# Kernel optimization log

Hardware: AMD Instinct MI355X
Metric: run time of the kernel (lower is better)

## Reference

```python
import jax, jax.numpy as jnp
import numpy as np

N_NEWS, N_ENT, N_TOP = 100000, 50000, 2000
D = 128
N_EDGES = 1600000
HID, OUT = 512, 128


def setup_inputs() -> dict:
    key = jax.random.key(0)
    ks = jax.random.split(key, 12)
    return {
        "news_feats": jax.random.normal(ks[0], (N_NEWS, D), jnp.float32),
        "entity_feats": jax.random.normal(ks[1], (N_ENT, D), jnp.float32),
        "topic_feats": jax.random.normal(ks[2], (N_TOP, D), jnp.float32),
        "ent_row": jax.random.randint(ks[3], (N_EDGES,), 0, N_NEWS, jnp.int32),
        "ent_col": jax.random.randint(ks[4], (N_EDGES,), 0, N_ENT, jnp.int32),
        "top_row": jax.random.randint(ks[5], (N_EDGES,), 0, N_NEWS, jnp.int32),
        "top_col": jax.random.randint(ks[6], (N_EDGES,), 0, N_TOP, jnp.int32),
        "W1": jax.random.normal(ks[7], (3 * D, HID), jnp.float32) * 0.05,
        "b1": jnp.zeros((HID,), jnp.float32),
        "W2": jax.random.normal(ks[8], (HID, OUT), jnp.float32) * 0.05,
        "b2": jnp.zeros((OUT,), jnp.float32),
    }


def _agg(feats, row, col, num_news):
    # SpMM with binary adjacency: sum neighbor feats per news node
    gathered = feats[col]                                   # [E, D]
    summed = jax.ops.segment_sum(gathered, row, num_segments=num_news)
    deg = jax.ops.segment_sum(jnp.ones_like(row, dtype=feats.dtype), row,
                              num_segments=num_news)
    return summed / (deg[:, None] + 1e-8)


def reference(news_feats, entity_feats, topic_feats, ent_row, ent_col,
              top_row, top_col, W1, b1, W2, b2):
    n = news_feats.shape[0]
    ent_agg = _agg(entity_feats, ent_row, ent_col, n)
    top_agg = _agg(topic_feats, top_row, top_col, n)
    out = jnp.concatenate([news_feats, ent_agg, top_agg], axis=1)  # [N, 3D]
    h = jnp.tanh(out @ W1 + b1)
    return h @ W2 + b2
```

## Files before the change

kernel.cpp:

```cpp
#include <hip/hip_runtime.h>
#include <hip/hip_bf16.h>

#define NN 100000
#define NE 50000
#define NT 2000
#define DD 128
#define NEDGE 1600000
#define HID 512
#define OUTD 128
#define K1 (3*DD)
#define NBKT 391

typedef __bf16 bf16x8 __attribute__((ext_vector_type(8)));
typedef __bf16 bf16x4 __attribute__((ext_vector_type(4)));
typedef float  f32x4  __attribute__((ext_vector_type(4)));

__device__ __forceinline__ __bf16 f2b(float f) {
    __hip_bfloat16 h = __float2bfloat16(f);
    union { __hip_bfloat16 h; __bf16 b; } u; u.h = h; return u.b;
}

__device__ __forceinline__ void gll16(const void* g, void* l) {
    __builtin_amdgcn_global_load_lds((const __attribute__((address_space(1))) void*)g,
                                     (__attribute__((address_space(3))) void*)l, 16, 0, 0);
}

__device__ __forceinline__ float ftanh(float x) {
    x = fminf(fmaxf(x, -15.f), 15.f);
    float t = __expf(2.f * x);
    return (t - 1.f) / (t + 1.f);
}

__global__ void conv_feats(const float* __restrict__ entf, const float* __restrict__ topf,
                           __bf16* __restrict__ entb, __bf16* __restrict__ topb) {
    long i = ((long)blockIdx.x * 256 + threadIdx.x) * 4;
    const long NEL = (long)NE * DD;
    if (i < NEL) {
        float4 v = *(const float4*)(entf + i);
        *(bf16x4*)(entb + i) = bf16x4{f2b(v.x), f2b(v.y), f2b(v.z), f2b(v.w)};
    } else {
        long j = i - NEL;
        float4 v = *(const float4*)(topf + j);
        *(bf16x4*)(topb + j) = bf16x4{f2b(v.x), f2b(v.y), f2b(v.z), f2b(v.w)};
    }
}

__global__ __launch_bounds__(256) void hist_buckets(const int* __restrict__ er,
                                                    const int* __restrict__ tr,
                                                    int* __restrict__ bc_e,
                                                    int* __restrict__ bc_t) {
    __shared__ int lhe[NBKT], lht[NBKT];
    const int tid = threadIdx.x;
    for (int i = tid; i < NBKT; i += 256) { lhe[i] = 0; lht[i] = 0; }
    __syncthreads();
    const int base = blockIdx.x * 8192;
    #pragma unroll 4
    for (int k = 0; k < 32; k++) {
        int e = base + k * 256 + tid;
        if (e < NEDGE) {
            atomicAdd(&lhe[er[e] >> 8], 1);
            atomicAdd(&lht[tr[e] >> 8], 1);
        }
    }
    __syncthreads();
    for (int i = tid; i < NBKT; i += 256) {
        if (lhe[i]) atomicAdd(&bc_e[i], lhe[i]);
        if (lht[i]) atomicAdd(&bc_t[i], lht[i]);
    }
}

__global__ void scan_buckets(int* __restrict__ bc_e, int* __restrict__ bc_t,
                             int* __restrict__ cur_e, int* __restrict__ cur_t,
                             int* __restrict__ offs_e, int* __restrict__ offs_t) {
    int* bc  = blockIdx.y ? bc_t : bc_e;
    int* cur = blockIdx.y ? cur_t : cur_e;
    int* offs = blockIdx.y ? offs_t : offs_e;
    __shared__ int s[512];
    int i = threadIdx.x;
    s[i] = (i < NBKT) ? bc[i] : 0;
    __syncthreads();
    #pragma unroll
    for (int off = 1; off < 512; off <<= 1) {
        int v = (i >= off) ? s[i - off] : 0;
        __syncthreads();
        s[i] += v;
        __syncthreads();
    }
    if (i < NBKT) {
        bc[i] = s[i];
        cur[i] = i ? s[i - 1] : 0;
    }
    if (i == 0) offs[0] = 0;
}

__global__ __launch_bounds__(256) void scatter_bucket(const int* __restrict__ er,
                                                      const int* __restrict__ ec,
                                                      const int* __restrict__ tr,
                                                      const int* __restrict__ tc,
                                                      int* __restrict__ cur_e,
                                                      int* __restrict__ cur_t,
                                                      int* __restrict__ be,
                                                      int* __restrict__ bt) {
    __shared__ int lhe[NBKT], lht[NBKT];
    __shared__ int lbe[NBKT], lbt[NBKT];
    const int tid = threadIdx.x;
    for (int i = tid; i < NBKT; i += 256) { lhe[i] = 0; lht[i] = 0; }
    __syncthreads();
    const int base = blockIdx.x * 4096;
    #pragma unroll 4
    for (int k = 0; k < 16; k++) {
        int e = base + k * 256 + tid;
        if (e < NEDGE) {
            atomicAdd(&lhe[er[e] >> 8], 1);
            atomicAdd(&lht[tr[e] >> 8], 1);
        }
    }
    __syncthreads();
    for (int i = tid; i < NBKT; i += 256) {
        int c = lhe[i];
        lbe[i] = c ? atomicAdd(&cur_e[i], c) : 0;
        lhe[i] = 0;
        c = lht[i];
        lbt[i] = c ? atomicAdd(&cur_t[i], c) : 0;
        lht[i] = 0;
    }
    __syncthreads();
    #pragma unroll 4
    for (int k = 0; k < 16; k++) {
        int e = base + k * 256 + tid;
        if (e < NEDGE) {
            int r = er[e];
            int b = r >> 8;
            int p = lbe[b] + atomicAdd(&lhe[b], 1);
            be[p] = ((r & 255) << 16) | ec[e];
            r = tr[e];
            b = r >> 8;
            p = lbt[b] + atomicAdd(&lht[b], 1);
            bt[p] = ((r & 255) << 16) | tc[e];
        }
    }
}

__global__ __launch_bounds__(256) void bucket_csr(const int* __restrict__ be,
                                                  const int* __restrict__ bt,
                                                  const int* __restrict__ bc_e,
                                                  const int* __restrict__ bc_t,
                                                  int* __restrict__ offs_e,
                                                  int* __restrict__ offs_t,
                                                  int* __restrict__ se,
                                                  int* __restrict__ st) {
    const int* buf = blockIdx.y ? bt : be;
    const int* bc  = blockIdx.y ? bc_t : bc_e;
    int* offs      = blockIdx.y ? offs_t : offs_e;
    int* sout      = blockIdx.y ? st : se;
    const int b = blockIdx.x;
    const int tid = threadIdx.x;
    const int start = b ? bc[b - 1] : 0;
    const int cnt = bc[b] - start;

    __shared__ int scn[256];
    __shared__ int lcur[256];
    scn[tid] = 0;
    __syncthreads();
    for (int i = tid; i < cnt; i += 256)
        atomicAdd(&scn[buf[start + i] >> 16], 1);
    __syncthreads();
    #pragma unroll
    for (int off = 1; off < 256; off <<= 1) {
        int v = (tid >= off) ? scn[tid - off] : 0;
        __syncthreads();
        scn[tid] += v;
        __syncthreads();
    }
    const int node = b * 256 + tid;
    if (node < NN) offs[node + 1] = start + scn[tid];
    lcur[tid] = start + (tid ? scn[tid - 1] : 0);
    __syncthreads();
    for (int i = tid; i < cnt; i += 256) {
        int v = buf[start + i];
        int p = atomicAdd(&lcur[v >> 16], 1);
        sout[p] = v & 0xFFFF;
    }
}

__global__ __launch_bounds__(256) void aggregate2(const float* __restrict__ news,
                                                  const __bf16* __restrict__ entb,
                                                  const __bf16* __restrict__ topb,
                                                  const int* __restrict__ offs_e,
                                                  const int* __restrict__ offs_t,
                                                  const int* __restrict__ se,
                                                  const int* __restrict__ st,
                                                  __bf16* __restrict__ X) {
    const int wave = threadIdx.x >> 6, lane = threadIdx.x & 63;
    const int node = blockIdx.x * 4 + wave;
    if (node >= NN) return;
    const int h = lane >> 4;
    const int d = (lane & 15) * 8;

    float ea[8] = {0,0,0,0,0,0,0,0};
    float pa[8] = {0,0,0,0,0,0,0,0};

    const int s0 = offs_e[node], s1 = offs_e[node + 1];
    int i = s0 + h;
    for (; i + 12 < s1; i += 16) {
        int c0 = se[i], c1 = se[i + 4], c2 = se[i + 8], c3 = se[i + 12];
        bf16x8 v0 = *(const bf16x8*)(entb + (long)c0 * DD + d);
        bf16x8 v1 = *(const bf16x8*)(entb + (long)c1 * DD + d);
        bf16x8 v2 = *(const bf16x8*)(entb + (long)c2 * DD + d);
        bf16x8 v3 = *(const bf16x8*)(entb + (long)c3 * DD + d);
        #pragma unroll
        for (int j = 0; j < 8; j++)
            ea[j] += ((float)v0[j] + (float)v1[j]) + ((float)v2[j] + (float)v3[j]);
    }
    for (; i < s1; i += 4) {
        bf16x8 v = *(const bf16x8*)(entb + (long)se[i] * DD + d);
        #pragma unroll
        for (int j = 0; j < 8; j++) ea[j] += (float)v[j];
    }

    const int t0 = offs_t[node], t1 = offs_t[node + 1];
    i = t0 + h;
    for (; i + 12 < t1; i += 16) {
        int c0 = st[i], c1 = st[i + 4], c2 = st[i + 8], c3 = st[i + 12];
        bf16x8 v0 = *(const bf16x8*)(topb + (long)c0 * DD + d);
        bf16x8 v1 = *(const bf16x8*)(topb + (long)c1 * DD + d);
        bf16x8 v2 = *(const bf16x8*)(topb + (long)c2 * DD + d);
        bf16x8 v3 = *(const bf16x8*)(topb + (long)c3 * DD + d);
        #pragma unroll
        for (int j = 0; j < 8; j++)
            pa[j] += ((float)v0[j] + (float)v1[j]) + ((float)v2[j] + (float)v3[j]);
    }
    for (; i < t1; i += 4) {
        bf16x8 v = *(const bf16x8*)(topb + (long)st[i] * DD + d);
        #pragma unroll
        for (int j = 0; j < 8; j++) pa[j] += (float)v[j];
    }

    #pragma unroll
    for (int j = 0; j < 8; j++) {
        ea[j] += __shfl_xor(ea[j], 16, 64);
        ea[j] += __shfl_xor(ea[j], 32, 64);
        pa[j] += __shfl_xor(pa[j], 16, 64);
        pa[j] += __shfl_xor(pa[j], 32, 64);
    }

    const float ie = 1.0f / ((float)(s1 - s0) + 1e-8f);
    const float it = 1.0f / ((float)(t1 - t0) + 1e-8f);
    __bf16* xr = X + (long)node * K1;
    if (h == 0) {
        float4 n0 = *(const float4*)(news + (long)node * DD + d);
        float4 n1 = *(const float4*)(news + (long)node * DD + d + 4);
        *(bf16x8*)(xr + d) = bf16x8{f2b(n0.x), f2b(n0.y), f2b(n0.z), f2b(n0.w),
                                    f2b(n1.x), f2b(n1.y), f2b(n1.z), f2b(n1.w)};
    } else if (h == 1) {
        *(bf16x8*)(xr + DD + d) = bf16x8{f2b(ea[0]*ie), f2b(ea[1]*ie), f2b(ea[2]*ie), f2b(ea[3]*ie),
                                         f2b(ea[4]*ie), f2b(ea[5]*ie), f2b(ea[6]*ie), f2b(ea[7]*ie)};
    } else if (h == 2) {
        *(bf16x8*)(xr + 2*DD + d) = bf16x8{f2b(pa[0]*it), f2b(pa[1]*it), f2b(pa[2]*it), f2b(pa[3]*it),
                                           f2b(pa[4]*it), f2b(pa[5]*it), f2b(pa[6]*it), f2b(pa[7]*it)};
    }
}

__global__ void conv_w(const float* __restrict__ W1, const float* __restrict__ W2,
                       __bf16* __restrict__ W1T, __bf16* __restrict__ W2T) {
    int i = blockIdx.x * 256 + threadIdx.x;
    if (i < K1 * HID) {
        int k = i / HID, n = i % HID;
        W1T[n * K1 + k] = f2b(W1[i]);
    } else {
        int j = i - K1 * HID;
        if (j < HID * OUTD) {
            int k = j / OUTD, n = j % OUTD;
            W2T[n * HID + k] = f2b(W2[j]);
        }
    }
}

template<int TANH>
__global__ __launch_bounds__(256) void gemm128(const __bf16* __restrict__ A,
                                               const __bf16* __restrict__ BT,
                                               const float* __restrict__ bias,
                                               void* __restrict__ Cout,
                                               int M, int N, int K) {
    __shared__ __bf16 As[128 * 32];
    __shared__ __bf16 Bs[128 * 32];
    const int bm = blockIdx.x * 128;
    const int bn = blockIdx.y * 128;
    const int t = threadIdx.x;
    const int lane = t & 63;
    const int w = t >> 6;
    const int quad = lane >> 4;
    const int l16 = lane & 15;
    const int wm = w >> 1, wn = w & 1;

    const int srow = w * 16 + (lane >> 2);
    const int skk = (lane & 3) * 8;

    f32x4 acc[4][4];
    #pragma unroll
    for (int i = 0; i < 4; i++)
        #pragma unroll
        for (int j = 0; j < 4; j++)
            #pragma unroll
            for (int r = 0; r < 4; r++) acc[i][j][r] = 0.0f;

    int ar0 = bm + srow;        if (ar0 >= M) ar0 = M - 1;
    int ar1 = bm + srow + 64;   if (ar1 >= M) ar1 = M - 1;
    const int br0 = bn + srow;
    const int br1 = bn + srow + 64;

    const int nk = K >> 5;
    for (int kt = 0; kt < nk; kt++) {
        const int k0 = kt << 5;
        __syncthreads();
        gll16(A  + (long)ar0 * K + k0 + skk, (void*)(As + w * 512));
        gll16(A  + (long)ar1 * K + k0 + skk, (void*)(As + 2048 + w * 512));
        gll16(BT + (long)br0 * K + k0 + skk, (void*)(Bs + w * 512));
        gll16(BT + (long)br1 * K + k0 + skk, (void*)(Bs + 2048 + w * 512));
        __syncthreads();
        bf16x8 af[4], bfr[4];
        #pragma unroll
        for (int i = 0; i < 4; i++) {
            af[i]  = *(const bf16x8*)&As[(wm * 64 + i * 16 + l16) * 32 + quad * 8];
            bfr[i] = *(const bf16x8*)&Bs[(wn * 64 + i * 16 + l16) * 32 + quad * 8];
        }
        #pragma unroll
        for (int i = 0; i < 4; i++)
            #pragma unroll
            for (int j = 0; j < 4; j++)
                acc[i][j] = __builtin_amdgcn_mfma_f32_16x16x32_bf16(af[i], bfr[j], acc[i][j], 0, 0, 0);
    }

    #pragma unroll
    for (int j = 0; j < 4; j++) {
        const int gc = bn + wn * 64 + j * 16 + l16;
        const float bb = bias[gc];
        #pragma unroll
        for (int i = 0; i < 4; i++) {
            const int rbase = bm + wm * 64 + i * 16 + quad * 4;
            #pragma unroll
            for (int r = 0; r < 4; r++) {
                const int gr = rbase + r;
                if (gr < M) {
                    float v = acc[i][j][r] + bb;
                    if (TANH) {
                        ((__bf16*)Cout)[(long)gr * N + gc] = f2b(ftanh(v));
                    } else {
                        ((float*)Cout)[(long)gr * N + gc] = v;
                    }
                }
            }
        }
    }
}

extern "C" void kernel_launch(void* const* d_in, const int* in_sizes, int n_in,
                              void* d_out, int out_size, void* d_ws, size_t ws_size,
                              hipStream_t stream) {
    const float* news  = (const float*)d_in[0];
    const float* ent_f = (const float*)d_in[1];
    const float* top_f = (const float*)d_in[2];
    const int* ent_row = (const int*)d_in[3];
    const int* ent_col = (const int*)d_in[4];
    const int* top_row = (const int*)d_in[5];
    const int* top_col = (const int*)d_in[6];
    const float* W1 = (const float*)d_in[7];
    const float* b1 = (const float*)d_in[8];
    const float* W2 = (const float*)d_in[9];
    const float* b2 = (const float*)d_in[10];

    char* ws = (char*)d_ws;
    int* offs_e = (int*)(ws + 0);
    int* offs_t = (int*)(ws + 400016);
    int* bc_e   = (int*)(ws + 800032);
    int* bc_t   = (int*)(ws + 801596);
    int* cur_e  = (int*)(ws + 803160);
    int* cur_t  = (int*)(ws + 804724);
    int* be     = (int*)(ws + 806320);
    int* bt     = (int*)(ws + 7206320);
    int* se     = (int*)(ws + 13606320);
    int* st     = (int*)(ws + 20006320);
    __bf16* entb = (__bf16*)(ws + 26406336);
    __bf16* topb = (__bf16*)(ws + 39206336);
    __bf16* H   = (__bf16*)(ws + 0);
    __bf16* X   = (__bf16*)(ws + 102400000);
    __bf16* W1T = (__bf16*)(ws + 179200000);
    __bf16* W2T = (__bf16*)(ws + 179593216);

    hipMemsetAsync(ws + 800032, 0, 6256, stream);
    conv_w<<<1024, 256, 0, stream>>>(W1, W2, W1T, W2T);
    conv_feats<<<6500, 256, 0, stream>>>(ent_f, top_f, entb, topb);
    hist_buckets<<<196, 256, 0, stream>>>(ent_row, top_row, bc_e, bc_t);
    scan_buckets<<<dim3(1, 2), 512, 0, stream>>>(bc_e, bc_t, cur_e, cur_t, offs_e, offs_t);
    scatter_bucket<<<392, 256, 0, stream>>>(ent_row, ent_col, top_row, top_col,
                                            cur_e, cur_t, be, bt);
    bucket_csr<<<dim3(NBKT, 2), 256, 0, stream>>>(be, bt, bc_e, bc_t,
                                                  offs_e, offs_t, se, st);
    aggregate2<<<NN / 4, 256, 0, stream>>>(news, entb, topb, offs_e, offs_t, se, st, X);
    gemm128<1><<<dim3(782, 4), 256, 0, stream>>>(X, W1T, b1, (void*)H, NN, HID, K1);
    gemm128<0><<<dim3(782, 1), 256, 0, stream>>>(H, W2T, b2, d_out, NN, OUTD, HID);
}
```

Before: 580.9 us.

## Fuse two MLP GEMMs into one kernel keeping hidden tile in LDS

Replaces the two GEMM launches with one kernel per 128-row block. It computes each 128-column chunk of the tanh hidden layer, stores it in LDS and immediately accumulates it into the output projection, so the bf16 hidden matrix never goes to global memory. It also adds XOR swizzling on the LDS tiles to cut bank conflicts. In exchange, each block re-stages the X tile once per hidden chunk, only 782 blocks run with a larger LDS footprint, and the per-chunk loops have more barriers.

```diff
diff --git a/kernel.cpp b/kernel.cpp
--- a/kernel.cpp
+++ b/kernel.cpp
@@ -276,16 +276,47 @@
     }
 }
 
-template<int TANH>
-__global__ __launch_bounds__(256) void gemm128(const __bf16* __restrict__ A,
-                                               const __bf16* __restrict__ BT,
-                                               const float* __restrict__ bias,
-                                               void* __restrict__ Cout,
-                                               int M, int N, int K) {
-    __shared__ __bf16 As[128 * 32];
-    __shared__ __bf16 Bs[128 * 32];
+
+__device__ __forceinline__ void stage_tile(const __bf16* __restrict__ src, int ldK,
+                                           int k0, int row0, int rowmax,
+                                           __bf16* lds, int w, int lane) {
+    #pragma unroll
+    for (int half = 0; half < 2; half++) {
+        int ss = w * 64 + half * 256 + lane;
+        int r = ss >> 2;
+        int sw = (r & 3) ^ ((r >> 2) & 3);
+        int c = (ss & 3) ^ sw;
+        int gr = row0 + r; if (gr >= rowmax) gr = rowmax - 1;
+        gll16(src + (long)gr * ldK + k0 + c * 8,
+              lds + (w * 64 + half * 256) * 8);
+    }
+}
+
+__device__ __forceinline__ bf16x8 frag(const __bf16* lds, int r, int q) {
+    int sw = (r & 3) ^ ((r >> 2) & 3);
+    return *(const bf16x8*)(lds + (r * 4 + (q ^ sw)) * 8);
+}
+
+__device__ __forceinline__ void hs_write(__bf16* Hs, int r, int c, __bf16 v) {
+    int ch = c >> 3;
+    int pch = ((((ch >> 2) ^ ((r >> 2) & 3)) << 2) | ((ch & 3) ^ (r & 3)));
+    Hs[(r * 16 + pch) * 8 + (c & 7)] = v;
+}
+__device__ __forceinline__ bf16x8 hs_frag(const __bf16* Hs, int r, int kk, int q) {
+    int pch = (((kk ^ ((r >> 2) & 3)) << 2) | (q ^ (r & 3)));
+    return *(const bf16x8*)(Hs + (r * 16 + pch) * 8);
+}
+
+__global__ __launch_bounds__(256, 2) void mlp_fused(const __bf16* __restrict__ X,
+                                                    const __bf16* __restrict__ W1T,
+                                                    const float* __restrict__ b1,
+                                                    const __bf16* __restrict__ W2T,
+                                                    const float* __restrict__ b2,
+                                                    float* __restrict__ out) {
+    __shared__ __bf16 Xs[128 * 32];
+    __shared__ __bf16 Ws[128 * 32];
+    __shared__ __bf16 Hs[128 * 128];
     const int bm = blockIdx.x * 128;
-    const int bn = blockIdx.y * 128;
     const int t = threadIdx.x;
     const int lane = t & 63;
     const int w = t >> 6;
@@ -293,62 +324,83 @@
     const int l16 = lane & 15;
     const int wm = w >> 1, wn = w & 1;
 
-    const int srow = w * 16 + (lane >> 2);
-    const int skk = (lane & 3) * 8;
-
-    f32x4 acc[4][4];
+    f32x4 oacc[4][4];
     #pragma unroll
     for (int i = 0; i < 4; i++)
         #pragma unroll
         for (int j = 0; j < 4; j++)
             #pragma unroll
-            for (int r = 0; r < 4; r++) acc[i][j][r] = 0.0f;
-
-    int ar0 = bm + srow;        if (ar0 >= M) ar0 = M - 1;
-    int ar1 = bm + srow + 64;   if (ar1 >= M) ar1 = M - 1;
-    const int br0 = bn + srow;
-    const int br1 = bn + srow + 64;
-
-    const int nk = K >> 5;
-    for (int kt = 0; kt < nk; kt++) {
-        const int k0 = kt << 5;
-        __syncthreads();
-        gll16(A  + (long)ar0 * K + k0 + skk, (void*)(As + w * 512));
-        gll16(A  + (long)ar1 * K + k0 + skk, (void*)(As + 2048 + w * 512));
-        gll16(BT + (long)br0 * K + k0 + skk, (void*)(Bs + w * 512));
-        gll16(BT + (long)br1 * K + k0 + skk, (void*)(Bs + 2048 + w * 512));
-        __syncthreads();
-        bf16x8 af[4], bfr[4];
-        #pragma unroll
-        for (int i = 0; i < 4; i++) {
-            af[i]  = *(const bf16x8*)&As[(wm * 64 + i * 16 + l16) * 32 + quad * 8];
-            bfr[i] = *(const bf16x8*)&Bs[(wn * 64 + i * 16 + l16) * 32 + quad * 8];
-        }
+            for (int r = 0; r < 4; r++) oacc[i][j][r] = 0.0f;
+
+    for (int nc = 0; nc < 4; nc++) {
+        f32x4 hacc[4][4];
         #pragma unroll
         for (int i = 0; i < 4; i++)
             #pragma unroll
             for (int j = 0; j < 4; j++)
-                acc[i][j] = __builtin_amdgcn_mfma_f32_16x16x32_bf16(af[i], bfr[j], acc[i][j], 0, 0, 0);
+                #pragma unroll
+                for (int r = 0; r < 4; r++) hacc[i][j][r] = 0.0f;
+
+        for (int kt = 0; kt < K1 / 32; kt++) {
+            __syncthreads();
+            stage_tile(X,   K1, kt * 32, bm,       NN,  Xs, w, lane);
+            stage_tile(W1T, K1, kt * 32, nc * 128, HID, Ws, w, lane);
+            __syncthreads();
+            bf16x8 af[4], bfr[4];
+            #pragma unroll
+            for (int i = 0; i < 4; i++) {
+                af[i]  = frag(Xs, wm * 64 + i * 16 + l16, quad);
+                bfr[i] = frag(Ws, wn * 64 + i * 16 + l16, quad);
+            }
+            #pragma unroll
+            for (int i = 0; i < 4; i++)
+                #pragma unroll
+                for (int j = 0; j < 4; j++)
+                    hacc[i][j] = __builtin_amdgcn_mfma_f32_16x16x32_bf16(af[i], bfr[j], hacc[i][j], 0, 0, 0);
+        }
+
+        #pragma unroll
+        for (int j = 0; j < 4; j++) {
+            const int col = wn * 64 + j * 16 + l16;
+            const float bb = b1[nc * 128 + col];
+            #pragma unroll
+            for (int i = 0; i < 4; i++) {
+                const int rbase = wm * 64 + i * 16 + quad * 4;
+                #pragma unroll
+                for (int r = 0; r < 4; r++)
+                    hs_write(Hs, rbase + r, col, f2b(ftanh(hacc[i][j][r] + bb)));
+            }
+        }
+
+        for (int kk = 0; kk < 4; kk++) {
+            __syncthreads();
+            stage_tile(W2T, HID, nc * 128 + kk * 32, 0, OUTD, Ws, w, lane);
+            __syncthreads();
+            bf16x8 af[4], bfr[4];
+            #pragma unroll
+            for (int i = 0; i < 4; i++) {
+                af[i]  = hs_frag(Hs, wm * 64 + i * 16 + l16, kk, quad);
+                bfr[i] = frag(Ws, wn * 64 + i * 16 + l16, quad);
+            }
+            #pragma unroll
+            for (int i = 0; i < 4; i++)
+                #pragma unroll
+                for (int j = 0; j < 4; j++)
+                    oacc[i][j] = __builtin_amdgcn_mfma_f32_16x16x32_bf16(af[i], bfr[j], oacc[i][j], 0, 0, 0);
+        }
     }
 
     #pragma unroll
     for (int j = 0; j < 4; j++) {
-        const int gc = bn + wn * 64 + j * 16 + l16;
-        const float bb = bias[gc];
+        const int gc = wn * 64 + j * 16 + l16;
+        const float bb = b2[gc];
         #pragma unroll
         for (int i = 0; i < 4; i++) {
             const int rbase = bm + wm * 64 + i * 16 + quad * 4;
             #pragma unroll
             for (int r = 0; r < 4; r++) {
                 const int gr = rbase + r;
-                if (gr < M) {
-                    float v = acc[i][j][r] + bb;
-                    if (TANH) {
-                        ((__bf16*)Cout)[(long)gr * N + gc] = f2b(ftanh(v));
-                    } else {
-                        ((float*)Cout)[(long)gr * N + gc] = v;
-                    }
-                }
+                if (gr < NN) out[(long)gr * OUTD + gc] = oacc[i][j][r] + bb;
             }
         }
     }
@@ -382,7 +434,6 @@
     int* st     = (int*)(ws + 20006320);
     __bf16* entb = (__bf16*)(ws + 26406336);
     __bf16* topb = (__bf16*)(ws + 39206336);
-    __bf16* H   = (__bf16*)(ws + 0);
     __bf16* X   = (__bf16*)(ws + 102400000);
     __bf16* W1T = (__bf16*)(ws + 179200000);
     __bf16* W2T = (__bf16*)(ws + 179593216);
@@ -397,6 +448,5 @@
     bucket_csr<<<dim3(NBKT, 2), 256, 0, stream>>>(be, bt, bc_e, bc_t,
                                                   offs_e, offs_t, se, st);
     aggregate2<<<NN / 4, 256, 0, stream>>>(news, entb, topb, offs_e, offs_t, se, st, X);
-    gemm128<1><<<dim3(782, 4), 256, 0, stream>>>(X, W1T, b1, (void*)H, NN, HID, K1);
-    gemm128<0><<<dim3(782, 1), 256, 0, stream>>>(H, W2T, b2, d_out, NN, OUTD, HID);
-}
+    mlp_fused<<<782, 256, 0, stream>>>(X, W1T, b1, W2T, b2, (float*)d_out);
+}
```

After: 530.6 us. 8.7% less time.
